# Kernel tuning notes

Measured on AMD Instinct MI355X. Metric: run time of the kernel, lower is better.

Reference implementation:

```python
import jax, jax.numpy as jnp
import numpy as np

B, N, K, C, C_OUT = 8, 4096, 16, 192, 192
BN_EPS = 1e-5


def setup_inputs() -> dict:
    key = jax.random.key(0)
    k1, k2, k3, k4 = jax.random.split(key, 4)
    x = jax.random.normal(k1, (B, N, C), dtype=jnp.float32)
    edge_index = jax.random.randint(k2, (B, N, K), 0, N)
    # Linear(2C -> C_out): store weight as [2C, C_out] (transposed torch layout)
    lim = 1.0 / np.sqrt(2 * C)
    W = jax.random.uniform(k3, (2 * C, C_OUT), minval=-lim, maxval=lim, dtype=jnp.float32)
    b = jax.random.uniform(k4, (C_OUT,), minval=-lim, maxval=lim, dtype=jnp.float32)
    gamma = jnp.ones((C_OUT,), dtype=jnp.float32)
    beta = jnp.zeros((C_OUT,), dtype=jnp.float32)
    return {"x": x, "W": W, "b": b, "gamma": gamma, "beta": beta, "edge_index": edge_index}


def reference(x, W, b, gamma, beta, edge_index):
    Bb, Nn, Cc = x.shape
    # gather neighbor features: neighbors[b,n,k,:] = x[b, edge_index[b,n,k], :]
    batch_idx = jnp.arange(Bb)[:, None, None]          # [B,1,1]
    neighbors = x[batch_idx, edge_index]               # [B,N,K,C]
    # max-relative aggregation: max_k (x_j - x_i)
    agg = jnp.max(neighbors - x[:, :, None, :], axis=2)  # [B,N,C]
    h = jnp.concatenate([x, agg], axis=-1).reshape(Bb * Nn, 2 * Cc)
    # Linear
    y = h @ W + b                                      # [B*N, C_out]
    # BatchNorm1d (training-mode forward: batch stats, biased variance)
    mean = jnp.mean(y, axis=0)
    var = jnp.var(y, axis=0)
    y = (y - mean) * jax.lax.rsqrt(var + BN_EPS) * gamma + beta
    # exact (erf) GELU, torch default
    y = jax.nn.gelu(y, approximate=False)
    return y.reshape(Bb, Nn, -1)
```

## Files before the change

kernel.cpp:

```cpp
#include <hip/hip_runtime.h>
#include <math.h>

#define BDIM 8
#define NDIM 4096
#define KNBR 16
#define CDIM 192
#define COUT 192
#define TWO_C 384
#define ROWS (BDIM * NDIM)
#define BN_EPS 1e-5f

#define BM 64
#define HS 392
#define KSTEPS 12
#define NTILES 12

typedef __attribute__((ext_vector_type(8))) short short8;
typedef __attribute__((ext_vector_type(4))) float f32x4;

__device__ __forceinline__ float bf2f(unsigned short u) {
    unsigned int x = ((unsigned int)u) << 16;
    return __builtin_bit_cast(float, x);
}
__device__ __forceinline__ unsigned short f2bf(float f) {
    unsigned int u = __builtin_bit_cast(unsigned int, f);
    u += 0x7FFFu + ((u >> 16) & 1u);
    return (unsigned short)(u >> 16);
}
__device__ __forceinline__ float gelu_exact(float v) {
    return 0.5f * v * (1.0f + erff(v * 0.70710678118654752440f));
}

__global__ __launch_bounds__(256)
void cvt_x(const float* __restrict__ x, unsigned short* __restrict__ xb, int n8) {
    int i = blockIdx.x * 256 + threadIdx.x;
    if (i >= n8) return;
    const float4* p = (const float4*)(x + (size_t)i * 8);
    float4 a = p[0], b = p[1];
    short8 o;
    o[0] = (short)f2bf(a.x); o[1] = (short)f2bf(a.y);
    o[2] = (short)f2bf(a.z); o[3] = (short)f2bf(a.w);
    o[4] = (short)f2bf(b.x); o[5] = (short)f2bf(b.y);
    o[6] = (short)f2bf(b.z); o[7] = (short)f2bf(b.w);
    *(short8*)(xb + (size_t)i * 8) = o;
}

__global__ __launch_bounds__(256)
void pack_w(const float* __restrict__ W, unsigned short* __restrict__ Wtp) {
    int tid = blockIdx.x * 256 + threadIdx.x;
    if (tid >= KSTEPS * NTILES * 64) return;
    int ks = tid / (NTILES * 64);
    int r  = tid % (NTILES * 64);
    int nt = r / 64;
    int l  = r % 64;
    int k0 = ks * 32 + ((l >> 4) << 3);
    int c  = nt * 16 + (l & 15);
    short8 o;
#pragma unroll
    for (int j = 0; j < 8; ++j)
        o[j] = (short)f2bf(W[(size_t)(k0 + j) * COUT + c]);
    *(short8*)(Wtp + (size_t)tid * 8) = o;
}

__global__ __launch_bounds__(192)
void mrconv_mfma(const unsigned short* __restrict__ xb,
                 const unsigned short* __restrict__ Wtp,
                 const int*   __restrict__ edge,
                 unsigned short* __restrict__ y,
                 float* __restrict__ stats)
{
    __shared__ unsigned short h[BM * HS];
    __shared__ int eidx[BM * KNBR];

    const int t     = threadIdx.x;
    const int bid   = blockIdx.x;
    const int batch = bid & 7;
    const int tile  = bid >> 3;
    const int row0  = tile * BM;

    const unsigned short* xbb = xb + (size_t)batch * NDIM * CDIM;
    const int* eb = edge + ((size_t)batch * NDIM + row0) * KNBR;

    for (int i = t; i < BM * KNBR; i += 192) eidx[i] = eb[i];
    __syncthreads();

    {
        const int cc = t % 24;
        const int sn = t / 24;
        for (int it = 0; it < 8; ++it) {
            const int ln = it * 8 + sn;
            const unsigned short* xr = xbb + (size_t)(row0 + ln) * CDIM + cc * 8;
            short8 xi8 = *(const short8*)xr;
            float xif[8], agg[8];
#pragma unroll
            for (int q = 0; q < 8; ++q) {
                xif[q] = bf2f((unsigned short)xi8[q]);
                agg[q] = -INFINITY;
            }
#pragma unroll
            for (int k = 0; k < KNBR; ++k) {
                const int j = eidx[ln * KNBR + k];
                short8 xj8 = *(const short8*)(xbb + (size_t)j * CDIM + cc * 8);
#pragma unroll
                for (int q = 0; q < 8; ++q)
                    agg[q] = fmaxf(agg[q], bf2f((unsigned short)xj8[q]) - xif[q]);
            }
            *(short8*)&h[ln * HS + cc * 8] = xi8;
            short8 a8;
#pragma unroll
            for (int q = 0; q < 8; ++q) a8[q] = (short)f2bf(agg[q]);
            *(short8*)&h[ln * HS + CDIM + cc * 8] = a8;
        }
    }
    __syncthreads();

    const int wv   = t >> 6;
    const int lane = t & 63;
    const int lrow = lane & 15;
    const int lk   = (lane >> 4) << 3;

    f32x4 acc[4][4];
#pragma unroll
    for (int mt = 0; mt < 4; ++mt)
#pragma unroll
        for (int nt = 0; nt < 4; ++nt)
            acc[mt][nt] = (f32x4){0.f, 0.f, 0.f, 0.f};

    for (int ks = 0; ks < KSTEPS; ++ks) {
        short8 bfr[4], afr[4];
#pragma unroll
        for (int nt = 0; nt < 4; ++nt) {
            const int ng = wv * 4 + nt;
            bfr[nt] = *(const short8*)(Wtp + (size_t)((ks * NTILES + ng) * 64 + lane) * 8);
        }
#pragma unroll
        for (int mt = 0; mt < 4; ++mt)
            afr[mt] = *(const short8*)&h[(mt * 16 + lrow) * HS + ks * 32 + lk];
#pragma unroll
        for (int mt = 0; mt < 4; ++mt)
#pragma unroll
            for (int nt = 0; nt < 4; ++nt)
                acc[mt][nt] = __builtin_amdgcn_mfma_f32_16x16x32_bf16(
                    afr[mt], bfr[nt], acc[mt][nt], 0, 0, 0);
    }

    const size_t growbase = (size_t)batch * NDIM + row0;
    const int rj = (lane >> 4) << 2;
#pragma unroll
    for (int mt = 0; mt < 4; ++mt) {
#pragma unroll
        for (int nt = 0; nt < 4; ++nt) {
            const int col = wv * 64 + nt * 16 + lrow;
#pragma unroll
            for (int j = 0; j < 4; ++j) {
                const size_t rr = growbase + mt * 16 + rj + j;
                y[rr * COUT + col] = f2bf(acc[mt][nt][j]);
            }
        }
    }

#pragma unroll
    for (int nt = 0; nt < 4; ++nt) {
        float s = 0.f, q = 0.f;
#pragma unroll
        for (int mt = 0; mt < 4; ++mt)
#pragma unroll
            for (int j = 0; j < 4; ++j) {
                const float v = acc[mt][nt][j];
                s += v; q += v * v;
            }
        s += __shfl_xor(s, 16); s += __shfl_xor(s, 32);
        q += __shfl_xor(q, 16); q += __shfl_xor(q, 32);
        if (lane < 16) {
            const int col = wv * 64 + nt * 16 + lane;
            atomicAdd(&stats[col], s);
            atomicAdd(&stats[COUT + col], q);
        }
    }
}

__global__ __launch_bounds__(256)
void bn_gelu(const unsigned short* __restrict__ y,
             const float* __restrict__ stats,
             const float* __restrict__ gamma,
             const float* __restrict__ beta,
             float* __restrict__ out)
{
    __shared__ float sscale[COUT];
    __shared__ float sshift[COUT];
    const int t = threadIdx.x;
    if (t < COUT) {
        const float inv  = 1.0f / (float)ROWS;
        const float mean = stats[t] * inv;
        const float var  = stats[COUT + t] * inv - mean * mean;
        const float rstd = rsqrtf(var + BN_EPS);
        const float sc   = rstd * gamma[t];
        sscale[t] = sc;
        sshift[t] = beta[t] - mean * sc;
    }
    __syncthreads();

    const int i = blockIdx.x * 256 + t;
    if (i >= ROWS * COUT / 8) return;
    short8 v = *(const short8*)(y + (size_t)i * 8);
    const int c0 = (i % 24) * 8;
    float4 o0, o1;
    o0.x = gelu_exact(fmaf(bf2f((unsigned short)v[0]), sscale[c0 + 0], sshift[c0 + 0]));
    o0.y = gelu_exact(fmaf(bf2f((unsigned short)v[1]), sscale[c0 + 1], sshift[c0 + 1]));
    o0.z = gelu_exact(fmaf(bf2f((unsigned short)v[2]), sscale[c0 + 2], sshift[c0 + 2]));
    o0.w = gelu_exact(fmaf(bf2f((unsigned short)v[3]), sscale[c0 + 3], sshift[c0 + 3]));
    o1.x = gelu_exact(fmaf(bf2f((unsigned short)v[4]), sscale[c0 + 4], sshift[c0 + 4]));
    o1.y = gelu_exact(fmaf(bf2f((unsigned short)v[5]), sscale[c0 + 5], sshift[c0 + 5]));
    o1.z = gelu_exact(fmaf(bf2f((unsigned short)v[6]), sscale[c0 + 6], sshift[c0 + 6]));
    o1.w = gelu_exact(fmaf(bf2f((unsigned short)v[7]), sscale[c0 + 7], sshift[c0 + 7]));
    float4* po = (float4*)(out + (size_t)i * 8);
    po[0] = o0;
    po[1] = o1;
}

extern "C" void kernel_launch(void* const* d_in, const int* in_sizes, int n_in,
                              void* d_out, int out_size, void* d_ws, size_t ws_size,
                              hipStream_t stream) {
    const float* x     = (const float*)d_in[0];
    const float* W     = (const float*)d_in[1];
    const float* gamma = (const float*)d_in[3];
    const float* beta  = (const float*)d_in[4];
    const int*   edge  = (const int*)d_in[5];
    float* out = (float*)d_out;

    unsigned short* xb16 = (unsigned short*)d_ws;
    unsigned short* y16  = xb16 + (size_t)ROWS * CDIM;
    unsigned short* Wtp  = y16 + (size_t)ROWS * COUT;
    float* stats = (float*)(Wtp + (size_t)KSTEPS * NTILES * 64 * 8);

    hipMemsetAsync(stats, 0, 2 * COUT * sizeof(float), stream);
    cvt_x <<<dim3((ROWS * CDIM / 8 + 255) / 256), dim3(256), 0, stream>>>(x, xb16, ROWS * CDIM / 8);
    pack_w<<<dim3(36), dim3(256), 0, stream>>>(W, Wtp);
    mrconv_mfma<<<dim3(ROWS / BM), dim3(192), 0, stream>>>(xb16, Wtp, edge, y16, stats);
    bn_gelu<<<dim3(ROWS * COUT / 8 / 256), dim3(256), 0, stream>>>(y16, stats, gamma, beta, out);
}
```

Baseline: 59.91 us.

## Fuse prep kernels, use four waves in mrconv, hoist subtraction out of max

Replaces the memset, x-conversion and weight-packing launches with one prep kernel. Its first block ranges pack W, one block zeroes the stats and the rest convert x to bf16. The main kernel now runs 256 threads, so each of four waves owns 48 output columns (3 N-tiles) instead of three waves owning 64. The gather loop now computes max over neighbours first and subtracts x_i once per element, which rounds slightly differently but is mathematically equivalent. The aim is fewer launches and more waves per block for latency hiding, at the cost of a lower MFMA-to-A-fragment reuse ratio per wave.

After: 49.72 us (median of 2 runs). 1.2x faster.

```diff
diff --git a/kernel.cpp b/kernel.cpp
--- a/kernel.cpp
+++ b/kernel.cpp
@@ -31,12 +31,35 @@
     return 0.5f * v * (1.0f + erff(v * 0.70710678118654752440f));
 }
 
+#define CVT_BLK0 37
 __global__ __launch_bounds__(256)
-void cvt_x(const float* __restrict__ x, unsigned short* __restrict__ xb, int n8) {
-    int i = blockIdx.x * 256 + threadIdx.x;
-    if (i >= n8) return;
+void prep(const float* __restrict__ x, const float* __restrict__ W,
+          unsigned short* __restrict__ xb, unsigned short* __restrict__ Wtp,
+          float* __restrict__ stats) {
+    const int bid = blockIdx.x;
+    const int t   = threadIdx.x;
+    if (bid < 36) {
+        const int tid = bid * 256 + t;
+        const int ks = tid / (NTILES * 64);
+        const int r  = tid % (NTILES * 64);
+        const int nt = r / 64;
+        const int l  = r % 64;
+        const int k0 = ks * 32 + ((l >> 4) << 3);
+        const int c  = nt * 16 + (l & 15);
+        short8 o;
+#pragma unroll
+        for (int j = 0; j < 8; ++j)
+            o[j] = (short)f2bf(W[(size_t)(k0 + j) * COUT + c]);
+        *(short8*)(Wtp + (size_t)tid * 8) = o;
+        return;
+    }
+    if (bid == 36) {
+        for (int s = t; s < 2 * COUT; s += 256) stats[s] = 0.0f;
+        return;
+    }
+    const int i = (bid - CVT_BLK0) * 256 + t;
     const float4* p = (const float4*)(x + (size_t)i * 8);
-    float4 a = p[0], b = p[1];
+    const float4 a = p[0], b = p[1];
     short8 o;
     o[0] = (short)f2bf(a.x); o[1] = (short)f2bf(a.y);
     o[2] = (short)f2bf(a.z); o[3] = (short)f2bf(a.w);
@@ -46,23 +69,6 @@
 }
 
 __global__ __launch_bounds__(256)
-void pack_w(const float* __restrict__ W, unsigned short* __restrict__ Wtp) {
-    int tid = blockIdx.x * 256 + threadIdx.x;
-    if (tid >= KSTEPS * NTILES * 64) return;
-    int ks = tid / (NTILES * 64);
-    int r  = tid % (NTILES * 64);
-    int nt = r / 64;
-    int l  = r % 64;
-    int k0 = ks * 32 + ((l >> 4) << 3);
-    int c  = nt * 16 + (l & 15);
-    short8 o;
-#pragma unroll
-    for (int j = 0; j < 8; ++j)
-        o[j] = (short)f2bf(W[(size_t)(k0 + j) * COUT + c]);
-    *(short8*)(Wtp + (size_t)tid * 8) = o;
-}
-
-__global__ __launch_bounds__(192)
 void mrconv_mfma(const unsigned short* __restrict__ xb,
                  const unsigned short* __restrict__ Wtp,
                  const int*   __restrict__ edge,
@@ -81,36 +87,31 @@
     const unsigned short* xbb = xb + (size_t)batch * NDIM * CDIM;
     const int* eb = edge + ((size_t)batch * NDIM + row0) * KNBR;
 
-    for (int i = t; i < BM * KNBR; i += 192) eidx[i] = eb[i];
+    for (int i = t; i < BM * KNBR; i += 256) eidx[i] = eb[i];
     __syncthreads();
 
-    {
-        const int cc = t % 24;
-        const int sn = t / 24;
-        for (int it = 0; it < 8; ++it) {
-            const int ln = it * 8 + sn;
-            const unsigned short* xr = xbb + (size_t)(row0 + ln) * CDIM + cc * 8;
-            short8 xi8 = *(const short8*)xr;
-            float xif[8], agg[8];
-#pragma unroll
-            for (int q = 0; q < 8; ++q) {
-                xif[q] = bf2f((unsigned short)xi8[q]);
-                agg[q] = -INFINITY;
-            }
-#pragma unroll
-            for (int k = 0; k < KNBR; ++k) {
-                const int j = eidx[ln * KNBR + k];
-                short8 xj8 = *(const short8*)(xbb + (size_t)j * CDIM + cc * 8);
-#pragma unroll
-                for (int q = 0; q < 8; ++q)
-                    agg[q] = fmaxf(agg[q], bf2f((unsigned short)xj8[q]) - xif[q]);
-            }
-            *(short8*)&h[ln * HS + cc * 8] = xi8;
-            short8 a8;
-#pragma unroll
-            for (int q = 0; q < 8; ++q) a8[q] = (short)f2bf(agg[q]);
-            *(short8*)&h[ln * HS + CDIM + cc * 8] = a8;
-        }
+    for (int it = 0; it < 6; ++it) {
+        const int idx = it * 256 + t;
+        const int cc  = idx % 24;
+        const int ln  = idx / 24;
+        const short8 xi8 = *(const short8*)(xbb + (size_t)(row0 + ln) * CDIM + cc * 8);
+        float mx[8];
+#pragma unroll
+        for (int q = 0; q < 8; ++q) mx[q] = -INFINITY;
+#pragma unroll
+        for (int k = 0; k < KNBR; ++k) {
+            const int j = eidx[ln * KNBR + k];
+            const short8 xj8 = *(const short8*)(xbb + (size_t)j * CDIM + cc * 8);
+#pragma unroll
+            for (int q = 0; q < 8; ++q)
+                mx[q] = fmaxf(mx[q], bf2f((unsigned short)xj8[q]));
+        }
+        short8 a8;
+#pragma unroll
+        for (int q = 0; q < 8; ++q)
+            a8[q] = (short)f2bf(mx[q] - bf2f((unsigned short)xi8[q]));
+        *(short8*)&h[ln * HS + cc * 8]        = xi8;
+        *(short8*)&h[ln * HS + CDIM + cc * 8] = a8;
     }
     __syncthreads();
 
@@ -119,18 +120,18 @@
     const int lrow = lane & 15;
     const int lk   = (lane >> 4) << 3;
 
-    f32x4 acc[4][4];
+    f32x4 acc[4][3];
 #pragma unroll
     for (int mt = 0; mt < 4; ++mt)
 #pragma unroll
-        for (int nt = 0; nt < 4; ++nt)
+        for (int nt = 0; nt < 3; ++nt)
             acc[mt][nt] = (f32x4){0.f, 0.f, 0.f, 0.f};
 
     for (int ks = 0; ks < KSTEPS; ++ks) {
-        short8 bfr[4], afr[4];
-#pragma unroll
-        for (int nt = 0; nt < 4; ++nt) {
-            const int ng = wv * 4 + nt;
+        short8 bfr[3], afr[4];
+#pragma unroll
+        for (int nt = 0; nt < 3; ++nt) {
+            const int ng = wv * 3 + nt;
             bfr[nt] = *(const short8*)(Wtp + (size_t)((ks * NTILES + ng) * 64 + lane) * 8);
         }
 #pragma unroll
@@ -139,7 +140,7 @@
 #pragma unroll
         for (int mt = 0; mt < 4; ++mt)
 #pragma unroll
-            for (int nt = 0; nt < 4; ++nt)
+            for (int nt = 0; nt < 3; ++nt)
                 acc[mt][nt] = __builtin_amdgcn_mfma_f32_16x16x32_bf16(
                     afr[mt], bfr[nt], acc[mt][nt], 0, 0, 0);
     }
@@ -149,8 +150,8 @@
 #pragma unroll
     for (int mt = 0; mt < 4; ++mt) {
 #pragma unroll
-        for (int nt = 0; nt < 4; ++nt) {
-            const int col = wv * 64 + nt * 16 + lrow;
+        for (int nt = 0; nt < 3; ++nt) {
+            const int col = wv * 48 + nt * 16 + lrow;
 #pragma unroll
             for (int j = 0; j < 4; ++j) {
                 const size_t rr = growbase + mt * 16 + rj + j;
@@ -160,7 +161,7 @@
     }
 
 #pragma unroll
-    for (int nt = 0; nt < 4; ++nt) {
+    for (int nt = 0; nt < 3; ++nt) {
         float s = 0.f, q = 0.f;
 #pragma unroll
         for (int mt = 0; mt < 4; ++mt)
@@ -172,7 +173,7 @@
         s += __shfl_xor(s, 16); s += __shfl_xor(s, 32);
         q += __shfl_xor(q, 16); q += __shfl_xor(q, 32);
         if (lane < 16) {
-            const int col = wv * 64 + nt * 16 + lane;
+            const int col = wv * 48 + nt * 16 + lane;
             atomicAdd(&stats[col], s);
             atomicAdd(&stats[COUT + col], q);
         }
@@ -201,7 +202,6 @@
     __syncthreads();
 
     const int i = blockIdx.x * 256 + t;
-    if (i >= ROWS * COUT / 8) return;
     short8 v = *(const short8*)(y + (size_t)i * 8);
     const int c0 = (i % 24) * 8;
     float4 o0, o1;
@@ -228,14 +228,12 @@
     const int*   edge  = (const int*)d_in[5];
     float* out = (float*)d_out;
 
-    unsigned short* xb16 = (unsigned short*)d_ws;
-    unsigned short* y16  = xb16 + (size_t)ROWS * CDIM;
-    unsigned short* Wtp  = y16 + (size_t)ROWS * COUT;
+    unsigned short* Wtp  = (unsigned short*)d_ws;
     float* stats = (float*)(Wtp + (size_t)KSTEPS * NTILES * 64 * 8);
-
-    hipMemsetAsync(stats, 0, 2 * COUT * sizeof(float), stream);
-    cvt_x <<<dim3((ROWS * CDIM / 8 + 255) / 256), dim3(256), 0, stream>>>(x, xb16, ROWS * CDIM / 8);
-    pack_w<<<dim3(36), dim3(256), 0, stream>>>(W, Wtp);
-    mrconv_mfma<<<dim3(ROWS / BM), dim3(192), 0, stream>>>(xb16, Wtp, edge, y16, stats);
+    unsigned short* y16  = (unsigned short*)(stats + 2 * COUT);
+    unsigned short* xb16 = y16 + (size_t)ROWS * COUT;
+
+    prep<<<dim3(CVT_BLK0 + ROWS * CDIM / 8 / 256), dim3(256), 0, stream>>>(x, W, xb16, Wtp, stats);
+    mrconv_mfma<<<dim3(ROWS / BM), dim3(256), 0, stream>>>(xb16, Wtp, edge, y16, stats);
     bn_gelu<<<dim3(ROWS * COUT / 8 / 256), dim3(256), 0, stream>>>(y16, stats, gamma, beta, out);
 }
```
